# Kernel tuning notes

Measured on AMD Instinct MI355X. Metric: run time of the kernel, lower is better.

Reference implementation:

```python
import jax, jax.numpy as jnp
import numpy as np

B, N, D = 4, 4096, 1024


def setup_inputs() -> dict:
    key = jax.random.key(0)
    ks = jax.random.split(key, 7)
    s = 1.0 / np.sqrt(D)
    return {
        "x": jax.random.normal(ks[0], (B, N, D), dtype=jnp.float32),
        "Wq": jax.random.uniform(ks[1], (D, D), jnp.float32, -s, s),
        "bq": jax.random.uniform(ks[2], (D,), jnp.float32, -s, s),
        "Wk": jax.random.uniform(ks[3], (D, D), jnp.float32, -s, s),
        "bk": jax.random.uniform(ks[4], (D,), jnp.float32, -s, s),
        "Wv": jax.random.uniform(ks[5], (D, D), jnp.float32, -s, s),
        "bv": jax.random.uniform(ks[6], (D,), jnp.float32, -s, s),
    }


def reference(x, Wq, bq, Wk, bk, Wv, bv):
    # Projections (nn.Linear: x @ W.T + b; here W stored as [in, out])
    Q = x @ Wq + bq
    K = x @ Wk + bk
    V = x @ Wv + bv
    Qp = jax.nn.elu(Q) + 1.0  # positive feature map
    Kp = jax.nn.elu(K) + 1.0
    KV = jnp.einsum('bnd,bne->bde', Kp, V)          # [B, D, D]
    numerator = jnp.einsum('bnd,bde->bne', Qp, KV)  # [B, N, D]
    K_sum = Kp.sum(axis=1)                           # [B, D]
    norm = jnp.einsum('bnd,bd->bn', Qp, K_sum)[..., None]
    eps = 1e-6
    return numerator / (norm + eps)
```

## Files before the change

kernel.cpp:

```cpp
#include <hip/hip_runtime.h>
#include <hip/hip_bf16.h>
#include <cstdint>

typedef __bf16 bf16x8 __attribute__((ext_vector_type(8)));
typedef float  f32x4  __attribute__((ext_vector_type(4)));
typedef unsigned short u16x8 __attribute__((ext_vector_type(8)));

__device__ __forceinline__ unsigned short f2bf(float f) {
  __hip_bfloat16 h = __float2bfloat16(f);
  return __builtin_bit_cast(unsigned short, h);
}
__device__ __forceinline__ float bf2f(unsigned short u) {
  return __builtin_bit_cast(float, (unsigned)u << 16);
}

#define GL2LDS16(gp, lp)                                                      \
  __builtin_amdgcn_global_load_lds(                                           \
      (const __attribute__((address_space(1))) unsigned int*)(gp),            \
      (__attribute__((address_space(3))) unsigned int*)(lp), 16, 0, 0)

#define SBAR                                                                  \
  {                                                                           \
    __builtin_amdgcn_s_barrier();                                             \
    __builtin_amdgcn_sched_barrier(0);                                        \
  }
#define WAITV(n)                                                              \
  {                                                                           \
    asm volatile("s_waitcnt vmcnt(" #n ")" ::: "memory");                     \
    __builtin_amdgcn_sched_barrier(0);                                        \
  }
#define WAITL0                                                                \
  {                                                                           \
    asm volatile("s_waitcnt lgkmcnt(0)" ::: "memory");                        \
    __builtin_amdgcn_sched_barrier(0);                                        \
  }

template <int MODE>
__global__ __launch_bounds__(512, 2) void gemm256(
    const unsigned short* __restrict__ A, long long lda, long long aOffZ,
    const unsigned short* __restrict__ B, long long ldb, long long bOffZ,
    void* __restrict__ C, long long ldc, long long cOffZ,
    const float* __restrict__ bias, const float* __restrict__ bias2,
    const float* __restrict__ norm, long long normOffZ, int K) {
  __shared__ __attribute__((aligned(16))) char lds[2 * 65536];
  const int t = threadIdx.x;
  const int wave = t >> 6, lane = t & 63;
  const int wm = wave >> 2, wn = wave & 3;
  const int fr = lane & 15, fq = lane >> 4;

  const int gx = gridDim.x, gy = gridDim.y;
  int flat = blockIdx.y * gx + blockIdx.x;
  const int total = gx * gy;
  if ((total & 7) == 0) flat = (flat & 7) * (total >> 3) + (flat >> 3);
  int bx, by;
  if (MODE == 1) {
    bx = flat / gy;
    by = flat - bx * gy;
  } else {
    bx = flat % gx;
    by = flat / gx;
  }
  const int m0 = by * 256, n0 = bx * 256;

  const long long z = blockIdx.z;
  long long aBase, bBase;
  if (MODE == 3) {
    const long long koff = (z & 3) * 4096 + (z >> 2) * 1024;
    aBase = koff;
    bBase = koff;
  } else {
    aBase = z * aOffZ;
    bBase = z * bOffZ;
  }
  const unsigned short* Az = A + aBase;
  const unsigned short* Bz = B + bBase;

  const unsigned short* gA[2];
  const unsigned short* gB[2];
#pragma unroll
  for (int c = 0; c < 2; ++c) {
    int d = c * 8192 + t * 16;
    int l = d ^ (((d >> 7) & 3) << 4);
    int row = l >> 6, kel = (l & 63) >> 1;
    gA[c] = Az + (long long)(m0 + row) * lda + kel;
    gB[c] = Bz + (long long)(n0 + row) * ldb + kel;
  }

  const int slotx = (fr >> 1) & 3;
  const int acore = wm * 8192 + fr * 64 + ((fq ^ slotx) << 4);
  const int bcore = wn * 4096 + fr * 64 + ((fq ^ slotx) << 4);

  f32x4 acc[8][4];
#pragma unroll
  for (int i = 0; i < 8; ++i)
#pragma unroll
    for (int j = 0; j < 4; ++j) acc[i][j] = (f32x4){0.f, 0.f, 0.f, 0.f};

  const int NT = K >> 6;

  auto stage_sub = [&](int tile, int which) {
    char* dst = lds + (tile & 1) * 65536 + which * 16384 + wave * 1024;
    const int kofs = (tile << 6) + ((which >> 1) << 5);
    if (which & 1) {
      GL2LDS16(gB[0] + kofs, dst);
      GL2LDS16(gB[1] + kofs, dst + 8192);
    } else {
      GL2LDS16(gA[0] + kofs, dst);
      GL2LDS16(gA[1] + kofs, dst + 8192);
    }
  };

  stage_sub(0, 0);
  stage_sub(0, 1);
  stage_sub(0, 2);
  stage_sub(0, 3);
  WAITV(4);
  SBAR;

  bf16x8 av[4], bv0[4], bv1[4];
  for (int tt = 0; tt < NT - 1; ++tt) {
    const char* bufp = lds + (tt & 1) * 65536;
#pragma unroll
    for (int i = 0; i < 4; ++i) {
      av[i] = *(const bf16x8*)(bufp + acore + i * 1024);
      bv0[i] = *(const bf16x8*)(bufp + 16384 + bcore + i * 1024);
    }
    stage_sub(tt + 1, 0);
    SBAR;
    WAITL0;
    __builtin_amdgcn_s_setprio(1);
#pragma unroll
    for (int mi = 0; mi < 4; ++mi)
#pragma unroll
      for (int ni = 0; ni < 4; ++ni)
        acc[mi][ni] = __builtin_amdgcn_mfma_f32_16x16x32_bf16(
            av[mi], bv0[ni], acc[mi][ni], 0, 0, 0);
    __builtin_amdgcn_s_setprio(0);
    SBAR;
#pragma unroll
    for (int i = 0; i < 4; ++i)
      av[i] = *(const bf16x8*)(bufp + acore + (4 + i) * 1024);
    stage_sub(tt + 1, 1);
    SBAR;
    WAITL0;
    __builtin_amdgcn_s_setprio(1);
#pragma unroll
    for (int mi = 0; mi < 4; ++mi)
#pragma unroll
      for (int ni = 0; ni < 4; ++ni)
        acc[4 + mi][ni] = __builtin_amdgcn_mfma_f32_16x16x32_bf16(
            av[mi], bv0[ni], acc[4 + mi][ni], 0, 0, 0);
    __builtin_amdgcn_s_setprio(0);
    WAITV(4);
    SBAR;
#pragma unroll
    for (int i = 0; i < 4; ++i) {
      av[i] = *(const bf16x8*)(bufp + 32768 + acore + i * 1024);
      bv1[i] = *(const bf16x8*)(bufp + 49152 + bcore + i * 1024);
    }
    stage_sub(tt + 1, 2);
    SBAR;
    WAITL0;
    __builtin_amdgcn_s_setprio(1);
#pragma unroll
    for (int mi = 0; mi < 4; ++mi)
#pragma unroll
      for (int ni = 0; ni < 4; ++ni)
        acc[mi][ni] = __builtin_amdgcn_mfma_f32_16x16x32_bf16(
            av[mi], bv1[ni], acc[mi][ni], 0, 0, 0);
    __builtin_amdgcn_s_setprio(0);
    SBAR;
#pragma unroll
    for (int i = 0; i < 4; ++i)
      av[i] = *(const bf16x8*)(bufp + 32768 + acore + (4 + i) * 1024);
    stage_sub(tt + 1, 3);
    SBAR;
    WAITL0;
    __builtin_amdgcn_s_setprio(1);
#pragma unroll
    for (int mi = 0; mi < 4; ++mi)
#pragma unroll
      for (int ni = 0; ni < 4; ++ni)
        acc[4 + mi][ni] = __builtin_amdgcn_mfma_f32_16x16x32_bf16(
            av[mi], bv1[ni], acc[4 + mi][ni], 0, 0, 0);
    __builtin_amdgcn_s_setprio(0);
    WAITV(4);
    SBAR;
  }

  {
    const char* bufp = lds + ((NT - 1) & 1) * 65536;
#pragma unroll
    for (int i = 0; i < 4; ++i) {
      av[i] = *(const bf16x8*)(bufp + acore + i * 1024);
      bv0[i] = *(const bf16x8*)(bufp + 16384 + bcore + i * 1024);
    }
    SBAR;
    WAITL0;
#pragma unroll
    for (int mi = 0; mi < 4; ++mi)
#pragma unroll
      for (int ni = 0; ni < 4; ++ni)
        acc[mi][ni] = __builtin_amdgcn_mfma_f32_16x16x32_bf16(
            av[mi], bv0[ni], acc[mi][ni], 0, 0, 0);
    SBAR;
#pragma unroll
    for (int i = 0; i < 4; ++i)
      av[i] = *(const bf16x8*)(bufp + acore + (4 + i) * 1024);
    SBAR;
    WAITL0;
#pragma unroll
    for (int mi = 0; mi < 4; ++mi)
#pragma unroll
      for (int ni = 0; ni < 4; ++ni)
        acc[4 + mi][ni] = __builtin_amdgcn_mfma_f32_16x16x32_bf16(
            av[mi], bv0[ni], acc[4 + mi][ni], 0, 0, 0);
    WAITV(0);
    SBAR;
#pragma unroll
    for (int i = 0; i < 4; ++i) {
      av[i] = *(const bf16x8*)(bufp + 32768 + acore + i * 1024);
      bv1[i] = *(const bf16x8*)(bufp + 49152 + bcore + i * 1024);
    }
    WAITL0;
#pragma unroll
    for (int mi = 0; mi < 4; ++mi)
#pragma unroll
      for (int ni = 0; ni < 4; ++ni)
        acc[mi][ni] = __builtin_amdgcn_mfma_f32_16x16x32_bf16(
            av[mi], bv1[ni], acc[mi][ni], 0, 0, 0);
#pragma unroll
    for (int i = 0; i < 4; ++i)
      av[i] = *(const bf16x8*)(bufp + 32768 + acore + (4 + i) * 1024);
    WAITL0;
#pragma unroll
    for (int mi = 0; mi < 4; ++mi)
#pragma unroll
      for (int ni = 0; ni < 4; ++ni)
        acc[4 + mi][ni] = __builtin_amdgcn_mfma_f32_16x16x32_bf16(
            av[mi], bv1[ni], acc[4 + mi][ni], 0, 0, 0);
  }

  const float* nrmz = (MODE == 4) ? (norm + z * normOffZ) : nullptr;
  float* Cf = (float*)C + z * cOffZ;
  unsigned short* Cu = (unsigned short*)C + z * cOffZ;
  const bool lower = (m0 < 1024);
#pragma unroll
  for (int mi = 0; mi < 8; ++mi) {
    const int rbase = m0 + wm * 128 + mi * 16 + fq * 4;
    float rb[4], nv[4];
#pragma unroll
    for (int j = 0; j < 4; ++j) {
      if (MODE == 1)
        rb[j] = lower ? bias[rbase + j] : bias2[rbase - 1024 + j];
      if (MODE == 4) nv[j] = nrmz[rbase + j];
    }
#pragma unroll
    for (int ni = 0; ni < 4; ++ni) {
      const int c = n0 + wn * 64 + ni * 16 + fr;
      float cb = 0.f;
      if (MODE == 0) cb = bias[c];
#pragma unroll
      for (int j = 0; j < 4; ++j) {
        float v = acc[mi][ni][j];
        if (MODE == 0) v += cb;
        if (MODE == 1) v += rb[j];
        if (MODE == 0 || (MODE == 1 && lower))
          v = (v > 0.f) ? v + 1.f : __expf(v);
        const long long ci = (long long)(rbase + j) * ldc + c;
        if (MODE == 4)
          Cf[ci] = v / nv[j];
        else
          Cu[ci] = f2bf(v);
      }
    }
  }
}

__global__ __launch_bounds__(256) void reduce_kvt(
    const unsigned short* __restrict__ P, unsigned short* __restrict__ KVt) {
  const long long i = ((long long)blockIdx.x * 256 + threadIdx.x) * 8;
  const int b = (int)(i >> 20);
  const long long ed = i & ((1ll << 20) - 1);
  float s[8] = {0.f, 0.f, 0.f, 0.f, 0.f, 0.f, 0.f, 0.f};
#pragma unroll
  for (int ks = 0; ks < 4; ++ks) {
    u16x8 v = *(const u16x8*)(P + ((long long)(ks * 4 + b) << 20) + ed);
#pragma unroll
    for (int j = 0; j < 8; ++j) s[j] += bf2f(v[j]);
  }
  u16x8 o;
#pragma unroll
  for (int j = 0; j < 8; ++j) o[j] = f2bf(s[j]);
  *(u16x8*)(KVt + i) = o;
}

__global__ __launch_bounds__(256) void transpose_w(
    const float* __restrict__ W, unsigned short* __restrict__ WT) {
  __shared__ float tile[32][33];
  const int tx = threadIdx.x & 31, ty = threadIdx.x >> 5;
  const int i0 = blockIdx.y * 32, o0 = blockIdx.x * 32;
#pragma unroll
  for (int s = 0; s < 32; s += 8)
    tile[ty + s][tx] = W[(long long)(i0 + ty + s) * 1024 + o0 + tx];
  __syncthreads();
#pragma unroll
  for (int s = 0; s < 32; s += 8)
    WT[(long long)(o0 + ty + s) * 1024 + i0 + tx] = f2bf(tile[tx][ty + s]);
}

__global__ __launch_bounds__(256) void convert_x(
    const float4* __restrict__ in, uint2* __restrict__ out, int n4) {
  const int stride = gridDim.x * blockDim.x;
  for (int i = blockIdx.x * blockDim.x + threadIdx.x; i < n4; i += stride) {
    float4 v = in[i];
    uint2 o;
    o.x = (unsigned)f2bf(v.x) | ((unsigned)f2bf(v.y) << 16);
    o.y = (unsigned)f2bf(v.z) | ((unsigned)f2bf(v.w) << 16);
    out[i] = o;
  }
}

__global__ __launch_bounds__(256) void ksum_kernel(
    const unsigned short* __restrict__ KpT, float* __restrict__ Ksum) {
  const int gw = (blockIdx.x * 256 + threadIdx.x) >> 6;
  const int lane = threadIdx.x & 63;
  const int d = gw >> 2, b = gw & 3;
  const unsigned short* p = KpT + (long long)d * 16384 + b * 4096 + lane * 8;
  float s = 0.f;
#pragma unroll
  for (int it = 0; it < 8; ++it) {
    u16x8 v = *(const u16x8*)(p + it * 512);
#pragma unroll
    for (int j = 0; j < 8; ++j) s += bf2f(v[j]);
  }
#pragma unroll
  for (int o = 32; o > 0; o >>= 1) s += __shfl_down(s, o, 64);
  if (lane == 0) Ksum[b * 1024 + d] = s;
}

__global__ __launch_bounds__(256) void norm_kernel(
    const unsigned short* __restrict__ Qp, const float* __restrict__ Ksum,
    float* __restrict__ nrm) {
  const int gw = (blockIdx.x * 256 + threadIdx.x) >> 6;
  const int lane = threadIdx.x & 63;
  const int b = gw >> 12;
  const unsigned short* q = Qp + (long long)gw * 1024 + lane * 8;
  const float* ks = Ksum + b * 1024 + lane * 8;
  float s = 0.f;
#pragma unroll
  for (int it = 0; it < 2; ++it) {
    u16x8 v = *(const u16x8*)(q + it * 512);
    float4 k0 = *(const float4*)(ks + it * 512);
    float4 k1 = *(const float4*)(ks + it * 512 + 4);
    s += bf2f(v[0]) * k0.x + bf2f(v[1]) * k0.y + bf2f(v[2]) * k0.z +
         bf2f(v[3]) * k0.w + bf2f(v[4]) * k1.x + bf2f(v[5]) * k1.y +
         bf2f(v[6]) * k1.z + bf2f(v[7]) * k1.w;
  }
#pragma unroll
  for (int o = 32; o > 0; o >>= 1) s += __shfl_down(s, o, 64);
  if (lane == 0) nrm[gw] = s + 1e-6f;
}

extern "C" void kernel_launch(void* const* d_in, const int* in_sizes, int n_in,
                              void* d_out, int out_size, void* d_ws,
                              size_t ws_size, hipStream_t stream) {
  const float* x  = (const float*)d_in[0];
  const float* Wq = (const float*)d_in[1];
  const float* bq = (const float*)d_in[2];
  const float* Wk = (const float*)d_in[3];
  const float* bk = (const float*)d_in[4];
  const float* Wv = (const float*)d_in[5];
  const float* bv = (const float*)d_in[6];
  float* out = (float*)d_out;

  const size_t MN = 16384ull * 1024ull;
  char* w = (char*)d_ws;
  unsigned short* xb  = (unsigned short*)w;  w += MN * 2;
  unsigned short* WT  = (unsigned short*)w;  w += 3ull * 1024 * 1024 * 2;
  unsigned short* Qp  = (unsigned short*)w;  w += MN * 2;
  unsigned short* KVb = (unsigned short*)w;  w += 2 * MN * 2;
  unsigned short* KVt = (unsigned short*)w;  w += 4ull * 1024 * 1024 * 2;
  float* Ksum = (float*)w;  w += 4ull * 1024 * 4;
  float* nrm  = (float*)w;  w += 16384ull * 4;
  unsigned short* Pkv = xb;
  unsigned short* KpT = KVb;
  unsigned short* VT  = KVb + MN;

  transpose_w<<<dim3(32, 32), 256, 0, stream>>>(Wq, WT);
  transpose_w<<<dim3(32, 32), 256, 0, stream>>>(Wk, WT + 1024 * 1024);
  transpose_w<<<dim3(32, 32), 256, 0, stream>>>(Wv, WT + 2 * 1024 * 1024);
  convert_x<<<2048, 256, 0, stream>>>((const float4*)x, (uint2*)xb,
                                      (int)(MN / 4));

  gemm256<0><<<dim3(4, 64, 1), 512, 0, stream>>>(
      xb, 1024, 0, WT, 1024, 0, Qp, 1024, 0, bq, nullptr, nullptr, 0, 1024);
  gemm256<1><<<dim3(64, 8, 1), 512, 0, stream>>>(
      WT + 1024 * 1024, 1024, 0, xb, 1024, 0, KVb, 16384, 0, bk, bv, nullptr,
      0, 1024);
  ksum_kernel<<<1024, 256, 0, stream>>>(KpT, Ksum);
  gemm256<3><<<dim3(4, 4, 16), 512, 0, stream>>>(
      VT, 16384, 0, KpT, 16384, 0, Pkv, 1024, 1024 * 1024, nullptr, nullptr,
      nullptr, 0, 1024);
  reduce_kvt<<<2048, 256, 0, stream>>>(Pkv, KVt);
  norm_kernel<<<4096, 256, 0, stream>>>(Qp, Ksum, nrm);
  gemm256<4><<<dim3(4, 16, 4), 512, 0, stream>>>(
      Qp, 1024, 4096ll * 1024, KVt, 1024, 1024 * 1024, out, 1024,
      4096ll * 1024, nullptr, nullptr, nrm, 4096, 1024);
}
```

Baseline: 250.9 us.

## Reassociate KV as (Kp^T x) Wv plus Ksum⊗bv to skip computing V

Uses KV = Kp^T(xWv + bv) = (Kp^T x)Wv + Ksum·bv^T, so the full N×D V projection is never formed. Instead it computes M = Kp^T x per batch, a small split-K GEMM of M with Wv, and adds the bias term in the reduction kernel. This cuts GEMM FLOPs, but it adds two bf16 transposes (x and Kp), an extra split-K GEMM and an extra reduction pass. The result is also rounded to bf16 at an additional intermediate (M).

Result: slower. 257.4 us (+2.6%).

```diff
diff --git a/kernel.cpp b/kernel.cpp
--- a/kernel.cpp
+++ b/kernel.cpp
@@ -40,8 +40,8 @@
     const unsigned short* __restrict__ A, long long lda, long long aOffZ,
     const unsigned short* __restrict__ B, long long ldb, long long bOffZ,
     void* __restrict__ C, long long ldc, long long cOffZ,
-    const float* __restrict__ bias, const float* __restrict__ bias2,
-    const float* __restrict__ norm, long long normOffZ, int K) {
+    const float* __restrict__ bias, const float* __restrict__ norm,
+    long long normOffZ, int K) {
   __shared__ __attribute__((aligned(16))) char lds[2 * 65536];
   const int t = threadIdx.x;
   const int wave = t >> 6, lane = t & 63;
@@ -52,14 +52,7 @@
   int flat = blockIdx.y * gx + blockIdx.x;
   const int total = gx * gy;
   if ((total & 7) == 0) flat = (flat & 7) * (total >> 3) + (flat >> 3);
-  int bx, by;
-  if (MODE == 1) {
-    bx = flat / gy;
-    by = flat - bx * gy;
-  } else {
-    bx = flat % gx;
-    by = flat / gx;
-  }
+  const int bx = flat % gx, by = flat / gx;
   const int m0 = by * 256, n0 = bx * 256;
 
   const long long z = blockIdx.z;
@@ -68,6 +61,9 @@
     const long long koff = (z & 3) * 4096 + (z >> 2) * 1024;
     aBase = koff;
     bBase = koff;
+  } else if (MODE == 5) {
+    aBase = (z >> 2) * 256;
+    bBase = (z & 3) * 1048576ll + (z >> 2) * 256;
   } else {
     aBase = z * aOffZ;
     bBase = z * bOffZ;
@@ -244,17 +240,13 @@
   const float* nrmz = (MODE == 4) ? (norm + z * normOffZ) : nullptr;
   float* Cf = (float*)C + z * cOffZ;
   unsigned short* Cu = (unsigned short*)C + z * cOffZ;
-  const bool lower = (m0 < 1024);
 #pragma unroll
   for (int mi = 0; mi < 8; ++mi) {
     const int rbase = m0 + wm * 128 + mi * 16 + fq * 4;
-    float rb[4], nv[4];
-#pragma unroll
-    for (int j = 0; j < 4; ++j) {
-      if (MODE == 1)
-        rb[j] = lower ? bias[rbase + j] : bias2[rbase - 1024 + j];
+    float nv[4];
+#pragma unroll
+    for (int j = 0; j < 4; ++j)
       if (MODE == 4) nv[j] = nrmz[rbase + j];
-    }
 #pragma unroll
     for (int ni = 0; ni < 4; ++ni) {
       const int c = n0 + wn * 64 + ni * 16 + fr;
@@ -263,10 +255,10 @@
 #pragma unroll
       for (int j = 0; j < 4; ++j) {
         float v = acc[mi][ni][j];
-        if (MODE == 0) v += cb;
-        if (MODE == 1) v += rb[j];
-        if (MODE == 0 || (MODE == 1 && lower))
+        if (MODE == 0) {
+          v += cb;
           v = (v > 0.f) ? v + 1.f : __expf(v);
+        }
         const long long ci = (long long)(rbase + j) * ldc + c;
         if (MODE == 4)
           Cf[ci] = v / nv[j];
@@ -277,8 +269,35 @@
   }
 }
 
+__global__ __launch_bounds__(256) void transpose_bf(
+    const unsigned short* __restrict__ in, unsigned short* __restrict__ out) {
+  __shared__ unsigned short tile[4096];
+  const int t = threadIdx.x;
+  const long long r0 = (long long)blockIdx.x * 64;
+  const long long c0 = (long long)blockIdx.y * 64;
+#pragma unroll
+  for (int it = 0; it < 2; ++it) {
+    const int id = it * 256 + t;
+    const int r = id >> 3, cc = id & 7;
+    const int pc = cc ^ ((r >> 3) & 7);
+    *(u16x8*)&tile[r * 64 + pc * 8] =
+        *(const u16x8*)&in[(r0 + r) * 1024 + c0 + cc * 8];
+  }
+  __syncthreads();
+#pragma unroll
+  for (int it = 0; it < 2; ++it) {
+    const int id = it * 256 + t;
+    const int c = id >> 3, r8 = (id & 7) * 8;
+    const int pc = (c >> 3) ^ (r8 >> 3);
+    u16x8 v;
+#pragma unroll
+    for (int j = 0; j < 8; ++j) v[j] = tile[(r8 + j) * 64 + pc * 8 + (c & 7)];
+    *(u16x8*)&out[(c0 + c) * 16384 + r0 + r8] = v;
+  }
+}
+
 __global__ __launch_bounds__(256) void reduce_kvt(
-    const unsigned short* __restrict__ P, unsigned short* __restrict__ KVt) {
+    const unsigned short* __restrict__ P, unsigned short* __restrict__ Out) {
   const long long i = ((long long)blockIdx.x * 256 + threadIdx.x) * 8;
   const int b = (int)(i >> 20);
   const long long ed = i & ((1ll << 20) - 1);
@@ -292,6 +311,28 @@
   u16x8 o;
 #pragma unroll
   for (int j = 0; j < 8; ++j) o[j] = f2bf(s[j]);
+  *(u16x8*)(Out + i) = o;
+}
+
+__global__ __launch_bounds__(256) void reduce_kvt_bias(
+    const unsigned short* __restrict__ P, const float* __restrict__ bv,
+    const float* __restrict__ Ksum, unsigned short* __restrict__ KVt) {
+  const long long i = ((long long)blockIdx.x * 256 + threadIdx.x) * 8;
+  const int b = (int)(i >> 20);
+  const long long ed = i & ((1ll << 20) - 1);
+  const int e = (int)(ed >> 10), d = (int)(ed & 1023);
+  float s[8] = {0.f, 0.f, 0.f, 0.f, 0.f, 0.f, 0.f, 0.f};
+#pragma unroll
+  for (int ks = 0; ks < 4; ++ks) {
+    u16x8 v = *(const u16x8*)(P + ((long long)(ks * 4 + b) << 20) + ed);
+#pragma unroll
+    for (int j = 0; j < 8; ++j) s[j] += bf2f(v[j]);
+  }
+  const float bve = bv[e];
+  const float* kp = Ksum + b * 1024 + d;
+  u16x8 o;
+#pragma unroll
+  for (int j = 0; j < 8; ++j) o[j] = f2bf(s[j] + bve * kp[j]);
   *(u16x8*)(KVt + i) = o;
 }
 
@@ -376,35 +417,47 @@
 
   const size_t MN = 16384ull * 1024ull;
   char* w = (char*)d_ws;
-  unsigned short* xb  = (unsigned short*)w;  w += MN * 2;
-  unsigned short* WT  = (unsigned short*)w;  w += 3ull * 1024 * 1024 * 2;
-  unsigned short* Qp  = (unsigned short*)w;  w += MN * 2;
-  unsigned short* KVb = (unsigned short*)w;  w += 2 * MN * 2;
-  unsigned short* KVt = (unsigned short*)w;  w += 4ull * 1024 * 1024 * 2;
+  unsigned short* R0 = (unsigned short*)w;  w += MN * 2;
+  unsigned short* WT = (unsigned short*)w;  w += 3ull * 1024 * 1024 * 2;
+  unsigned short* Qp = (unsigned short*)w;  w += MN * 2;
+  unsigned short* R3 = (unsigned short*)w;  w += MN * 2;
+  unsigned short* xbT = (unsigned short*)w;  w += MN * 2;
+  unsigned short* R5 = (unsigned short*)w;  w += 4ull * 1024 * 1024 * 2;
   float* Ksum = (float*)w;  w += 4ull * 1024 * 4;
   float* nrm  = (float*)w;  w += 16384ull * 4;
-  unsigned short* Pkv = xb;
-  unsigned short* KpT = KVb;
-  unsigned short* VT  = KVb + MN;
+
+  unsigned short* xb  = R0;
+  unsigned short* Kp  = R3;
+  unsigned short* KpT = R0;
+  unsigned short* Pm  = R3;
+  unsigned short* M   = R5;
+  unsigned short* Pk2 = R3;
+  unsigned short* KVt = R5;
 
   transpose_w<<<dim3(32, 32), 256, 0, stream>>>(Wq, WT);
   transpose_w<<<dim3(32, 32), 256, 0, stream>>>(Wk, WT + 1024 * 1024);
   transpose_w<<<dim3(32, 32), 256, 0, stream>>>(Wv, WT + 2 * 1024 * 1024);
   convert_x<<<2048, 256, 0, stream>>>((const float4*)x, (uint2*)xb,
                                       (int)(MN / 4));
+  transpose_bf<<<dim3(256, 16), 256, 0, stream>>>(xb, xbT);
 
   gemm256<0><<<dim3(4, 64, 1), 512, 0, stream>>>(
-      xb, 1024, 0, WT, 1024, 0, Qp, 1024, 0, bq, nullptr, nullptr, 0, 1024);
-  gemm256<1><<<dim3(64, 8, 1), 512, 0, stream>>>(
-      WT + 1024 * 1024, 1024, 0, xb, 1024, 0, KVb, 16384, 0, bk, bv, nullptr,
-      0, 1024);
+      xb, 1024, 0, WT, 1024, 0, Qp, 1024, 0, bq, nullptr, 0, 1024);
+  gemm256<0><<<dim3(4, 64, 1), 512, 0, stream>>>(
+      xb, 1024, 0, WT + 1024 * 1024, 1024, 0, Kp, 1024, 0, bk, nullptr, 0,
+      1024);
+  transpose_bf<<<dim3(256, 16), 256, 0, stream>>>(Kp, KpT);
   ksum_kernel<<<1024, 256, 0, stream>>>(KpT, Ksum);
   gemm256<3><<<dim3(4, 4, 16), 512, 0, stream>>>(
-      VT, 16384, 0, KpT, 16384, 0, Pkv, 1024, 1024 * 1024, nullptr, nullptr,
-      nullptr, 0, 1024);
-  reduce_kvt<<<2048, 256, 0, stream>>>(Pkv, KVt);
+      KpT, 16384, 0, xbT, 16384, 0, Pm, 1024, 1024 * 1024, nullptr, nullptr,
+      0, 1024);
+  reduce_kvt<<<2048, 256, 0, stream>>>(Pm, M);
+  gemm256<5><<<dim3(4, 4, 16), 512, 0, stream>>>(
+      WT + 2 * 1024 * 1024, 1024, 0, M, 1024, 0, Pk2, 1024, 1024 * 1024,
+      nullptr, nullptr, 0, 256);
+  reduce_kvt_bias<<<2048, 256, 0, stream>>>(Pk2, bv, Ksum, KVt);
   norm_kernel<<<4096, 256, 0, stream>>>(Qp, Ksum, nrm);
   gemm256<4><<<dim3(4, 16, 4), 512, 0, stream>>>(
       Qp, 1024, 4096ll * 1024, KVt, 1024, 1024 * 1024, out, 1024,
-      4096ll * 1024, nullptr, nullptr, nrm, 4096, 1024);
-}
+      4096ll * 1024, nullptr, nrm, 4096, 1024);
+}
```

## Use 16-wave 256x256 GEMM with BK=32 triple-buffered LDS for projection GEMMs

Applied to the files above, without the earlier changes.

Adds a new projection GEMM kernel with 1024 threads (16 waves), each wave owning a 64x64 sub-tile. It streams K in 32-wide slices through three 32 KB LDS buffers instead of double-buffered 64 KB halves. The numerator GEMM moves into a separate specialised kernel that keeps the original 8-wave schedule. The aim is more latency hiding through more waves and a deeper prefetch pipeline. In exchange it needs more barriers per unit of work, and the aggressive launch bounds may squeeze the register budget.

Result: faster. 244.4 us (-2.6%).

```diff
diff --git a/kernel.cpp b/kernel.cpp
--- a/kernel.cpp
+++ b/kernel.cpp
@@ -36,13 +36,13 @@
   }
 
 template <int MODE>
-__global__ __launch_bounds__(512, 2) void gemm256(
+__global__ __launch_bounds__(1024, 4) void gemm256w(
     const unsigned short* __restrict__ A, long long lda, long long aOffZ,
     const unsigned short* __restrict__ B, long long ldb, long long bOffZ,
     void* __restrict__ C, long long ldc, long long cOffZ,
     const float* __restrict__ bias, const float* __restrict__ bias2,
-    const float* __restrict__ norm, long long normOffZ, int K) {
-  __shared__ __attribute__((aligned(16))) char lds[2 * 65536];
+    int K) {
+  __shared__ __attribute__((aligned(16))) char lds[3 * 32768];
   const int t = threadIdx.x;
   const int wave = t >> 6, lane = t & 63;
   const int wm = wave >> 2, wn = wave & 3;
@@ -75,6 +75,145 @@
   const unsigned short* Az = A + aBase;
   const unsigned short* Bz = B + bBase;
 
+  const unsigned short* gA;
+  const unsigned short* gB;
+  {
+    int d = t * 16;
+    int l = d ^ (((d >> 7) & 3) << 4);
+    int row = l >> 6, kel = (l & 63) >> 1;
+    gA = Az + (long long)(m0 + row) * lda + kel;
+    gB = Bz + (long long)(n0 + row) * ldb + kel;
+  }
+
+  const int slotx = (fr >> 1) & 3;
+  const int acore = wm * 4096 + fr * 64 + ((fq ^ slotx) << 4);
+  const int bcore = 16384 + wn * 4096 + fr * 64 + ((fq ^ slotx) << 4);
+
+  f32x4 acc[4][4];
+#pragma unroll
+  for (int i = 0; i < 4; ++i)
+#pragma unroll
+    for (int j = 0; j < 4; ++j) acc[i][j] = (f32x4){0.f, 0.f, 0.f, 0.f};
+
+  const int NT = K >> 5;
+
+  auto stage = [&](int tile) {
+    char* sb = lds + (tile % 3) * 32768 + wave * 1024;
+    const int k0 = tile << 5;
+    GL2LDS16(gA + k0, sb);
+    GL2LDS16(gB + k0, sb + 16384);
+  };
+
+  stage(0);
+  stage(1);
+  WAITV(2);
+  SBAR;
+
+  bf16x8 av[4], bv[4];
+  for (int tt = 0; tt < NT - 2; ++tt) {
+    const char* sb = lds + (tt % 3) * 32768;
+    stage(tt + 2);
+#pragma unroll
+    for (int i = 0; i < 4; ++i) {
+      av[i] = *(const bf16x8*)(sb + acore + i * 1024);
+      bv[i] = *(const bf16x8*)(sb + bcore + i * 1024);
+    }
+    WAITL0;
+    __builtin_amdgcn_s_setprio(1);
+#pragma unroll
+    for (int mi = 0; mi < 4; ++mi)
+#pragma unroll
+      for (int ni = 0; ni < 4; ++ni)
+        acc[mi][ni] = __builtin_amdgcn_mfma_f32_16x16x32_bf16(
+            av[mi], bv[ni], acc[mi][ni], 0, 0, 0);
+    __builtin_amdgcn_s_setprio(0);
+    WAITV(2);
+    SBAR;
+  }
+  {
+    const char* sb = lds + ((NT - 2) % 3) * 32768;
+#pragma unroll
+    for (int i = 0; i < 4; ++i) {
+      av[i] = *(const bf16x8*)(sb + acore + i * 1024);
+      bv[i] = *(const bf16x8*)(sb + bcore + i * 1024);
+    }
+    WAITL0;
+#pragma unroll
+    for (int mi = 0; mi < 4; ++mi)
+#pragma unroll
+      for (int ni = 0; ni < 4; ++ni)
+        acc[mi][ni] = __builtin_amdgcn_mfma_f32_16x16x32_bf16(
+            av[mi], bv[ni], acc[mi][ni], 0, 0, 0);
+    WAITV(0);
+    SBAR;
+  }
+  {
+    const char* sb = lds + ((NT - 1) % 3) * 32768;
+#pragma unroll
+    for (int i = 0; i < 4; ++i) {
+      av[i] = *(const bf16x8*)(sb + acore + i * 1024);
+      bv[i] = *(const bf16x8*)(sb + bcore + i * 1024);
+    }
+    WAITL0;
+#pragma unroll
+    for (int mi = 0; mi < 4; ++mi)
+#pragma unroll
+      for (int ni = 0; ni < 4; ++ni)
+        acc[mi][ni] = __builtin_amdgcn_mfma_f32_16x16x32_bf16(
+            av[mi], bv[ni], acc[mi][ni], 0, 0, 0);
+  }
+
+  unsigned short* Cu = (unsigned short*)C + z * cOffZ;
+  const bool lower = (m0 < 1024);
+#pragma unroll
+  for (int mi = 0; mi < 4; ++mi) {
+    const int rbase = m0 + wm * 64 + mi * 16 + fq * 4;
+    float rb[4];
+#pragma unroll
+    for (int j = 0; j < 4; ++j)
+      if (MODE == 1) rb[j] = lower ? bias[rbase + j] : bias2[rbase - 1024 + j];
+#pragma unroll
+    for (int ni = 0; ni < 4; ++ni) {
+      const int c = n0 + wn * 64 + ni * 16 + fr;
+      float cb = 0.f;
+      if (MODE == 0) cb = bias[c];
+#pragma unroll
+      for (int j = 0; j < 4; ++j) {
+        float v = acc[mi][ni][j];
+        if (MODE == 0) v += cb;
+        if (MODE == 1) v += rb[j];
+        if (MODE == 0 || (MODE == 1 && lower))
+          v = (v > 0.f) ? v + 1.f : __expf(v);
+        Cu[(long long)(rbase + j) * ldc + c] = f2bf(v);
+      }
+    }
+  }
+}
+
+__global__ __launch_bounds__(512, 2) void gemm_num(
+    const unsigned short* __restrict__ A, long long aOffZ,
+    const unsigned short* __restrict__ B, long long bOffZ,
+    float* __restrict__ C, long long cOffZ,
+    const float* __restrict__ norm, long long normOffZ) {
+  const long long lda = 1024, ldb = 1024, ldc = 1024;
+  const int K = 1024;
+  __shared__ __attribute__((aligned(16))) char lds[2 * 65536];
+  const int t = threadIdx.x;
+  const int wave = t >> 6, lane = t & 63;
+  const int wm = wave >> 2, wn = wave & 3;
+  const int fr = lane & 15, fq = lane >> 4;
+
+  const int gx = gridDim.x, gy = gridDim.y;
+  int flat = blockIdx.y * gx + blockIdx.x;
+  const int total = gx * gy;
+  if ((total & 7) == 0) flat = (flat & 7) * (total >> 3) + (flat >> 3);
+  const int bx = flat % gx, by = flat / gx;
+  const int m0 = by * 256, n0 = bx * 256;
+
+  const long long z = blockIdx.z;
+  const unsigned short* Az = A + z * aOffZ;
+  const unsigned short* Bz = B + z * bOffZ;
+
   const unsigned short* gA[2];
   const unsigned short* gB[2];
 #pragma unroll
@@ -187,7 +326,6 @@
     WAITV(4);
     SBAR;
   }
-
   {
     const char* bufp = lds + ((NT - 1) & 1) * 65536;
 #pragma unroll
@@ -241,38 +379,20 @@
             av[mi], bv1[ni], acc[4 + mi][ni], 0, 0, 0);
   }
 
-  const float* nrmz = (MODE == 4) ? (norm + z * normOffZ) : nullptr;
-  float* Cf = (float*)C + z * cOffZ;
-  unsigned short* Cu = (unsigned short*)C + z * cOffZ;
-  const bool lower = (m0 < 1024);
+  const float* nrmz = norm + z * normOffZ;
+  float* Cf = C + z * cOffZ;
 #pragma unroll
   for (int mi = 0; mi < 8; ++mi) {
     const int rbase = m0 + wm * 128 + mi * 16 + fq * 4;
-    float rb[4], nv[4];
-#pragma unroll
-    for (int j = 0; j < 4; ++j) {
-      if (MODE == 1)
-        rb[j] = lower ? bias[rbase + j] : bias2[rbase - 1024 + j];
-      if (MODE == 4) nv[j] = nrmz[rbase + j];
-    }
+    float nv[4];
+#pragma unroll
+    for (int j = 0; j < 4; ++j) nv[j] = nrmz[rbase + j];
 #pragma unroll
     for (int ni = 0; ni < 4; ++ni) {
       const int c = n0 + wn * 64 + ni * 16 + fr;
-      float cb = 0.f;
-      if (MODE == 0) cb = bias[c];
-#pragma unroll
-      for (int j = 0; j < 4; ++j) {
-        float v = acc[mi][ni][j];
-        if (MODE == 0) v += cb;
-        if (MODE == 1) v += rb[j];
-        if (MODE == 0 || (MODE == 1 && lower))
-          v = (v > 0.f) ? v + 1.f : __expf(v);
-        const long long ci = (long long)(rbase + j) * ldc + c;
-        if (MODE == 4)
-          Cf[ci] = v / nv[j];
-        else
-          Cu[ci] = f2bf(v);
-      }
+#pragma unroll
+      for (int j = 0; j < 4; ++j)
+        Cf[(long long)(rbase + j) * ldc + c] = acc[mi][ni][j] / nv[j];
     }
   }
 }
@@ -393,18 +513,16 @@
   convert_x<<<2048, 256, 0, stream>>>((const float4*)x, (uint2*)xb,
                                       (int)(MN / 4));
 
-  gemm256<0><<<dim3(4, 64, 1), 512, 0, stream>>>(
-      xb, 1024, 0, WT, 1024, 0, Qp, 1024, 0, bq, nullptr, nullptr, 0, 1024);
-  gemm256<1><<<dim3(64, 8, 1), 512, 0, stream>>>(
-      WT + 1024 * 1024, 1024, 0, xb, 1024, 0, KVb, 16384, 0, bk, bv, nullptr,
-      0, 1024);
+  gemm256w<0><<<dim3(4, 64, 1), 1024, 0, stream>>>(
+      xb, 1024, 0, WT, 1024, 0, Qp, 1024, 0, bq, nullptr, 1024);
+  gemm256w<1><<<dim3(64, 8, 1), 1024, 0, stream>>>(
+      WT + 1024 * 1024, 1024, 0, xb, 1024, 0, KVb, 16384, 0, bk, bv, 1024);
   ksum_kernel<<<1024, 256, 0, stream>>>(KpT, Ksum);
-  gemm256<3><<<dim3(4, 4, 16), 512, 0, stream>>>(
+  gemm256w<3><<<dim3(4, 4, 16), 1024, 0, stream>>>(
       VT, 16384, 0, KpT, 16384, 0, Pkv, 1024, 1024 * 1024, nullptr, nullptr,
-      nullptr, 0, 1024);
+      1024);
   reduce_kvt<<<2048, 256, 0, stream>>>(Pkv, KVt);
   norm_kernel<<<4096, 256, 0, stream>>>(Qp, Ksum, nrm);
-  gemm256<4><<<dim3(4, 16, 4), 512, 0, stream>>>(
-      Qp, 1024, 4096ll * 1024, KVt, 1024, 1024 * 1024, out, 1024,
-      4096ll * 1024, nullptr, nullptr, nrm, 4096, 1024);
-}
+  gemm_num<<<dim3(4, 16, 4), 512, 0, stream>>>(
+      Qp, 4096ll * 1024, KVt, 1024 * 1024, out, 4096ll * 1024, nrm, 4096);
+}
```
